# Optimization experiments

Hardware: AMD Instinct MI355X
Metric: run time of the kernel (lower is better)

Reference implementation:

```python
import jax, jax.numpy as jnp
import numpy as np

D_STATE = 16
D_CONV = 4


def layer_norm(x, g, b, eps=1e-5):
    mu = jnp.mean(x, axis=-1, keepdims=True)
    var = jnp.mean(jnp.square(x - mu), axis=-1, keepdims=True)
    return (x - mu) * jax.lax.rsqrt(var + eps) * g + b


def silu(x):
    return x * jax.nn.sigmoid(x)


def mamba(x, in_w, conv_w, conv_b, xproj_w, dt_w, dt_b, Alog, Dp, out_w):
    # x: [B, L, d_model]; in_w: [2*di, d_model]; conv_w: [di, d_conv]
    Bsz, L, _ = x.shape
    di = Dp.shape[0]
    xz = jnp.einsum('bld,ed->ble', x, in_w)          # [B,L,2*di]
    xs, z = jnp.split(xz, 2, axis=-1)
    # causal depthwise conv over L
    xt = xs.transpose(0, 2, 1)                        # [B,di,L]
    xt = jax.lax.conv_general_dilated(
        xt, conv_w[:, None, :], (1,), [(D_CONV - 1, 0)],
        feature_group_count=di, dimension_numbers=('NCH', 'OIH', 'NCH'))
    xs = silu((xt + conv_b[None, :, None]).transpose(0, 2, 1))  # [B,L,di]
    # input-dependent dt, B, C
    dbl = jnp.einsum('bld,ed->ble', xs, xproj_w)      # [B,L,dt_rank+2*ds]
    dt_rank = dt_w.shape[1]
    dt, Bc, Cc = jnp.split(dbl, [dt_rank, dt_rank + D_STATE], axis=-1)
    dt = jax.nn.softplus(jnp.einsum('blr,dr->bld', dt, dt_w) + dt_b)  # [B,L,di]
    A = -jnp.exp(Alog)                                # [di,ds]
    dA = jnp.exp(dt[..., None] * A)                   # [B,L,di,ds]
    dBx = dt[..., None] * Bc[:, :, None, :] * xs[..., None]  # [B,L,di,ds]

    def step(h, inp):
        dA_t, dBx_t, C_t = inp                        # [B,di,ds],[B,di,ds],[B,ds]
        h = dA_t * h + dBx_t
        y = jnp.einsum('bds,bs->bd', h, C_t)
        return h, y

    h0 = jnp.zeros((Bsz, di, D_STATE), x.dtype)
    _, ys = jax.lax.scan(step, h0, (dA.transpose(1, 0, 2, 3),
                                    dBx.transpose(1, 0, 2, 3),
                                    Cc.transpose(1, 0, 2)))
    y = ys.transpose(1, 0, 2) + Dp * xs               # [B,L,di]
    y = y * silu(z)
    return jnp.einsum('bld,od->blo', y, out_w)        # [B,L,d_model]


def _make_mamba_params(key, d_model, scale=0.02):
    di = 2 * d_model
    dt_rank = (d_model + 15) // 16
    ks = jax.random.split(key, 7)
    in_w = jax.random.normal(ks[0], (2 * di, d_model), jnp.float32) * scale
    conv_w = jax.random.normal(ks[1], (di, D_CONV), jnp.float32) * scale
    conv_b = jnp.zeros((di,), jnp.float32)
    xproj_w = jax.random.normal(ks[2], (dt_rank + 2 * D_STATE, di), jnp.float32) * scale
    dt_w = jax.random.normal(ks[3], (di, dt_rank), jnp.float32) * scale
    dt_b = jax.random.uniform(ks[4], (di,), jnp.float32, -5.0, -2.0)
    Alog = jnp.log(jnp.tile(jnp.arange(1, D_STATE + 1, dtype=jnp.float32), (di, 1)))
    Dp = jnp.ones((di,), jnp.float32)
    out_w = jax.random.normal(ks[5], (d_model, di), jnp.float32) * scale
    return in_w, conv_w, conv_b, xproj_w, dt_w, dt_b, Alog, Dp, out_w


def setup_inputs() -> dict:
    key = jax.random.key(0)
    B, L, D = 4, 2048, 1024
    DFF = 4 * D
    ks = jax.random.split(key, 8)
    x = jax.random.normal(ks[0], (B, L, D), jnp.float32)
    m1 = _make_mamba_params(ks[1], D)
    m2 = _make_mamba_params(ks[2], D)
    names1 = ['m1_in_w', 'm1_conv_w', 'm1_conv_b', 'm1_xproj_w', 'm1_dt_w', 'm1_dt_b', 'm1_Alog', 'm1_D', 'm1_out_w']
    names2 = ['m2_in_w', 'm2_conv_w', 'm2_conv_b', 'm2_xproj_w', 'm2_dt_w', 'm2_dt_b', 'm2_Alog', 'm2_D', 'm2_out_w']
    inp = {'x': x}
    inp.update(dict(zip(names1, m1)))
    inp.update(dict(zip(names2, m2)))
    inp['norm_g'] = jnp.ones((D,), jnp.float32)
    inp['norm_b'] = jnp.zeros((D,), jnp.float32)
    inp['ffn_g'] = jnp.ones((D,), jnp.float32)
    inp['ffn_b'] = jnp.zeros((D,), jnp.float32)
    inp['ff1_w'] = jax.random.normal(ks[3], (DFF, D), jnp.float32) * 0.02
    inp['ff1_b'] = jnp.zeros((DFF,), jnp.float32)
    inp['ff2_w'] = jax.random.normal(ks[4], (D, DFF), jnp.float32) * 0.02
    inp['ff2_b'] = jnp.zeros((D,), jnp.float32)
    return inp


def reference(x,
              m1_in_w, m1_conv_w, m1_conv_b, m1_xproj_w, m1_dt_w, m1_dt_b, m1_Alog, m1_D, m1_out_w,
              m2_in_w, m2_conv_w, m2_conv_b, m2_xproj_w, m2_dt_w, m2_dt_b, m2_Alog, m2_D, m2_out_w,
              norm_g, norm_b, ffn_g, ffn_b, ff1_w, ff1_b, ff2_w, ff2_b):
    # BiDirectionalAddBlock (dropout/droppath = identity in eval)
    h = layer_norm(x, norm_g, norm_b)
    fwd = mamba(h, m1_in_w, m1_conv_w, m1_conv_b, m1_xproj_w, m1_dt_w, m1_dt_b, m1_Alog, m1_D, m1_out_w)
    bwd = mamba(h[:, ::-1], m2_in_w, m2_conv_w, m2_conv_b, m2_xproj_w, m2_dt_w, m2_dt_b, m2_Alog, m2_D, m2_out_w)
    block_out = jax.nn.gelu(fwd + bwd + x, approximate=False)  # note: original does NOT flip bwd back
    x = x + block_out
    # FeedForward
    hf = layer_norm(x, ffn_g, ffn_b)
    hf = jax.nn.gelu(jnp.einsum('bld,hd->blh', hf, ff1_w) + ff1_b, approximate=False)
    x = x + jnp.einsum('blh,dh->bld', hf, ff2_w) + ff2_b
    return x
```

## Files before the change

### kernel.cpp

```cpp
#include <hip/hip_runtime.h>
#include <cmath>


namespace {

using u16 = unsigned short;
using uint = unsigned int;

constexpr int kB = 4;
constexpr int kL = 2048;
constexpr int kD = 1024;
constexpr int kDI = 2048;
constexpr int kDFF = 4096;
constexpr int kDS = 16;
constexpr int kDtRank = 64;
constexpr int kNPad = 128;
constexpr int kM = kB * kL;
constexpr int kNCH = 64;

typedef short bf16x8 __attribute__((ext_vector_type(8)));
typedef float f32x4  __attribute__((ext_vector_type(4)));

__device__ __forceinline__ float bf2f(u16 u) {
  union { unsigned int i; float f; } c; c.i = ((unsigned int)u) << 16; return c.f;
}
__device__ __forceinline__ u16 f2bf(float f) {
  union { float f; unsigned int i; } c; c.f = f;
  return (u16)((c.i + 0x7FFFu + ((c.i >> 16) & 1u)) >> 16);
}
__device__ __forceinline__ float geluf(float v) {
  return 0.5f * v * (1.f + erff(v * 0.70710678118654752f));
}
__device__ __forceinline__ float softplusf(float v) {
  return (v > 0.f) ? (v + log1pf(__expf(-v))) : log1pf(__expf(v));
}
__device__ __forceinline__ float siluf(float v) {
  return v / (1.f + __expf(-v));
}
__device__ __forceinline__ float exp2_fast(float v) {
  return __builtin_amdgcn_exp2f(v);
}

__device__ __forceinline__ void async16(const u16* g, u16* l) {
  __builtin_amdgcn_global_load_lds(
      (const __attribute__((address_space(1))) uint*)g,
      (__attribute__((address_space(3))) uint*)l, 16, 0, 0);
}

__global__ __launch_bounds__(256) void ln_kernel(
    const float* __restrict__ x, const float* __restrict__ g,
    const float* __restrict__ b, u16* __restrict__ out) {
  const int row = blockIdx.x;
  const int tid = threadIdx.x;
  const float4 v = ((const float4*)(x + (size_t)row * kD))[tid];
  float s  = v.x + v.y + v.z + v.w;
  float ss = v.x * v.x + v.y * v.y + v.z * v.z + v.w * v.w;
  #pragma unroll
  for (int off = 32; off; off >>= 1) {
    s  += __shfl_xor(s, off);
    ss += __shfl_xor(ss, off);
  }
  __shared__ float ls[4], lss[4];
  const int wid = tid >> 6;
  if ((tid & 63) == 0) { ls[wid] = s; lss[wid] = ss; }
  __syncthreads();
  s  = ls[0] + ls[1] + ls[2] + ls[3];
  ss = lss[0] + lss[1] + lss[2] + lss[3];
  const float mu  = s * (1.f / kD);
  const float inv = rsqrtf(ss * (1.f / kD) - mu * mu + 1e-5f);
  const float4 gg = ((const float4*)g)[tid];
  const float4 bb = ((const float4*)b)[tid];
  ushort4 o;
  o.x = f2bf((v.x - mu) * inv * gg.x + bb.x);
  o.y = f2bf((v.y - mu) * inv * gg.y + bb.y);
  o.z = f2bf((v.z - mu) * inv * gg.z + bb.z);
  o.w = f2bf((v.w - mu) * inv * gg.w + bb.w);
  ((ushort4*)(out + (size_t)row * kD))[tid] = o;
}

__global__ __launch_bounds__(256) void cvt_kernel(
    const float* __restrict__ s, u16* __restrict__ d) {
  const int i = blockIdx.x * 256 + threadIdx.x;
  const float4 v = ((const float4*)s)[i];
  ushort4 o = { f2bf(v.x), f2bf(v.y), f2bf(v.z), f2bf(v.w) };
  ((ushort4*)d)[i] = o;
}

__global__ __launch_bounds__(256) void cvt_xproj_kernel(
    const float* __restrict__ s, u16* __restrict__ d) {
  const int i = blockIdx.x * 256 + threadIdx.x;
  const int r = (i * 4) / kDI;
  ushort4 o = {0, 0, 0, 0};
  if (r < kDtRank + 2 * kDS) {
    const float4 v = ((const float4*)s)[i];
    o.x = f2bf(v.x); o.y = f2bf(v.y); o.z = f2bf(v.z); o.w = f2bf(v.w);
  }
  ((ushort4*)d)[i] = o;
}

template <int ACT, bool BIAS, bool ACC, bool OUTBF, bool REV, bool AMAP,
          bool CMAP>
__global__ __launch_bounds__(256) void gemm_mfma(
    const u16* __restrict__ A, int lda,
    const u16* __restrict__ W, int ldw,
    void* __restrict__ Cp, int ldc, int K,
    const float* __restrict__ bias, int seg_len, int row_off) {
  __shared__ __align__(16) u16 As[128][64];
  __shared__ __align__(16) u16 Ws[128][64];
  const int tid  = threadIdx.x;
  const int bm   = blockIdx.x * 128;
  const int bn   = blockIdx.y * 128;
  const int lane = tid & 63;
  const int wv   = tid >> 6;
  const int wm   = (wv >> 1) * 64;
  const int wn   = (wv & 1) * 64;
  const int l15  = lane & 15;
  const int quad = lane >> 4;
  const int srow = lane >> 3;
  const int swz  = ((lane & 7) ^ srow) * 8;
  const int jx   = (l15 & 7) * 16;

  int ab = 0, all0 = bm;
  if (AMAP || CMAP) {
    ab = bm / seg_len;
    all0 = bm - ab * seg_len;
  }

  int arowv[4];
  #pragma unroll
  for (int it = 0; it < 4; it++) {
    const int rl = it * 32 + wv * 8 + srow;
    if (AMAP) {
      arowv[it] = REV ? (ab * kL + kL - 1 - row_off - all0 - rl)
                      : (ab * kL + row_off + all0 + rl);
    } else {
      arowv[it] = bm + rl;
    }
  }

  f32x4 acc[4][4];
  #pragma unroll
  for (int i = 0; i < 4; i++)
    #pragma unroll
    for (int j = 0; j < 4; j++) acc[i][j] = (f32x4){0.f, 0.f, 0.f, 0.f};

  for (int k0 = 0; k0 < K; k0 += 64) {
    #pragma unroll
    for (int it = 0; it < 4; it++) {
      const int rl = it * 32 + wv * 8 + srow;
      async16(A + (size_t)arowv[it] * lda + k0 + swz, &As[it * 32 + wv * 8][0]);
      async16(W + (size_t)(bn + rl) * ldw + k0 + swz, &Ws[it * 32 + wv * 8][0]);
    }
    __syncthreads();
    #pragma unroll
    for (int ks = 0; ks < 64; ks += 32) {
      const int cb = ((ks >> 3) + quad) * 16;
      bf16x8 af[4], wf[4];
      #pragma unroll
      for (int i = 0; i < 4; i++)
        af[i] = *(const bf16x8*)((const char*)&As[wm + i * 16 + l15][0] +
                                 (cb ^ jx));
      #pragma unroll
      for (int j = 0; j < 4; j++)
        wf[j] = *(const bf16x8*)((const char*)&Ws[wn + j * 16 + l15][0] +
                                 (cb ^ jx));
      #pragma unroll
      for (int i = 0; i < 4; i++)
        #pragma unroll
        for (int j = 0; j < 4; j++)
          acc[i][j] = __builtin_amdgcn_mfma_f32_16x16x32_bf16(
              af[i], wf[j], acc[i][j], 0, 0, 0);
    }
    __syncthreads();
  }

  #pragma unroll
  for (int i = 0; i < 4; i++) {
    #pragma unroll
    for (int j = 0; j < 4; j++) {
      const int col = bn + wn + j * 16 + l15;
      #pragma unroll
      for (int r = 0; r < 4; r++) {
        const int rl2 = wm + i * 16 + quad * 4 + r;
        const int crow = CMAP ? (ab * kL + row_off + all0 + rl2) : (bm + rl2);
        float v = acc[i][j][r];
        if (BIAS) v += bias[col];
        if (ACT == 1) v = softplusf(v);
        if (ACT == 2) v = geluf(v);
        if (OUTBF) {
          ((u16*)Cp)[(size_t)crow * ldc + col] = f2bf(v);
        } else {
          float* p = (float*)Cp + (size_t)crow * ldc + col;
          if (ACC) *p = *p + v; else *p = v;
        }
      }
    }
  }
}

__global__ __launch_bounds__(256) void conv_silu_kernel(
    const u16* __restrict__ xz, const float* __restrict__ w,
    const float* __restrict__ cb, u16* __restrict__ xs,
    const u16* __restrict__ tail_in, u16* __restrict__ tail_out,
    int seg_len, int row_off) {
  const int t = blockIdx.x * 256 + threadIdx.x;
  const int c = t & (kDI - 1);
  const int r = t >> 11;
  const int b = r / seg_len;
  const int ll = r - b * seg_len;
  const int tpos = row_off + ll;

  const float xv0 = bf2f(xz[(size_t)r * (2 * kDI) + c]);
  float acc = cb[c] + w[c * 4 + 3] * xv0;
  #pragma unroll
  for (int j = 1; j <= 3; j++) {
    if (tpos - j >= 0) {
      float xp;
      if (ll - j >= 0) {
        xp = bf2f(xz[(size_t)(r - j) * (2 * kDI) + c]);
      } else {
        xp = bf2f(tail_in[(b * 3 + (3 + ll - j)) * kDI + c]);
      }
      acc += w[c * 4 + 3 - j] * xp;
    }
  }
  xs[(size_t)r * kDI + c] = f2bf(siluf(acc));
  if (ll >= seg_len - 3) {
    tail_out[(b * 3 + (ll - (seg_len - 3))) * kDI + c] = f2bf(xv0);
  }
}

__global__ __launch_bounds__(256, 8) void scan_phaseA(
    const u16* __restrict__ dt, const u16* __restrict__ xs,
    const u16* __restrict__ dbl, const float* __restrict__ Alog,
    float* __restrict__ Pbuf, float* __restrict__ Hbuf,
    int Lseg, int Lc) {
  __shared__ float Bls[32][16];
  const int tid = threadIdx.x;
  const int c = blockIdx.x * 256 + tid;
  const int k = blockIdx.y;
  const int b = blockIdx.z;
  const int base = b * Lseg + k * Lc;
  for (int idx = tid; idx < Lc * 16; idx += 256) {
    const int r = idx >> 4, j = idx & 15;
    Bls[r][j] = bf2f(dbl[(size_t)(base + r) * kNPad + kDtRank + j]);
  }
  __syncthreads();
  float Ac[16], h[16];
  float dtsum = 0.f;
  #pragma unroll
  for (int s = 0; s < 16; s++) {
    Ac[s] = -__expf(Alog[c * kDS + s]) * 1.44269504088896f;
    h[s] = 0.f;
  }
  for (int r = 0; r < Lc; r++) {
    const size_t row = (size_t)(base + r);
    const float dtv = bf2f(dt[row * kDI + c]);
    const float dtx = dtv * bf2f(xs[row * kDI + c]);
    dtsum += dtv;
    const float4* Brow = (const float4*)Bls[r];
    #pragma unroll
    for (int s4 = 0; s4 < 4; s4++) {
      const float4 Bv = Brow[s4];
      const float bb[4] = {Bv.x, Bv.y, Bv.z, Bv.w};
      #pragma unroll
      for (int q = 0; q < 4; q++) {
        const int s = s4 * 4 + q;
        const float dA = exp2_fast(dtv * Ac[s]);
        h[s] = dA * h[s] + dtx * bb[q];
      }
    }
  }
  const size_t o = (((size_t)b * kNCH + k) * kDI + c) * 16;
  #pragma unroll
  for (int s4 = 0; s4 < 4; s4++) {
    *(float4*)&Pbuf[o + s4 * 4] =
        make_float4(exp2_fast(Ac[s4 * 4 + 0] * dtsum),
                    exp2_fast(Ac[s4 * 4 + 1] * dtsum),
                    exp2_fast(Ac[s4 * 4 + 2] * dtsum),
                    exp2_fast(Ac[s4 * 4 + 3] * dtsum));
    *(float4*)&Hbuf[o + s4 * 4] =
        make_float4(h[s4 * 4], h[s4 * 4 + 1], h[s4 * 4 + 2], h[s4 * 4 + 3]);
  }
}

__global__ __launch_bounds__(256) void scan_phaseB(
    float* __restrict__ Pbuf, const float* __restrict__ Hbuf,
    float* __restrict__ hstate, int first) {
  const int t = blockIdx.x * 256 + threadIdx.x;
  const int s = t & 15;
  const int c = (t >> 4) & (kDI - 1);
  const int b = t >> 15;
  float cur = first ? 0.f : hstate[t];
  for (int k = 0; k < kNCH; k++) {
    const size_t idx = (((size_t)b * kNCH + k) * kDI + c) * 16 + s;
    const float p = Pbuf[idx];
    const float hl = Hbuf[idx];
    Pbuf[idx] = cur;
    cur = p * cur + hl;
  }
  hstate[t] = cur;
}

__global__ __launch_bounds__(256, 8) void scan_phaseC(
    const u16* __restrict__ dt, u16* __restrict__ xs,
    const u16* __restrict__ dbl, const u16* __restrict__ xz,
    const float* __restrict__ Alog, const float* __restrict__ Dp,
    const float* __restrict__ Pbuf, int Lseg, int Lc) {
  __shared__ float BC[32][32];
  const int tid = threadIdx.x;
  const int c = blockIdx.x * 256 + tid;
  const int k = blockIdx.y;
  const int b = blockIdx.z;
  const int base = b * Lseg + k * Lc;
  for (int idx = tid; idx < Lc * 32; idx += 256) {
    const int r = idx >> 5, j = idx & 31;
    BC[r][j] = bf2f(dbl[(size_t)(base + r) * kNPad + kDtRank + j]);
  }
  __syncthreads();
  float Ac[16], h[16];
  const size_t o = (((size_t)b * kNCH + k) * kDI + c) * 16;
  #pragma unroll
  for (int s4 = 0; s4 < 4; s4++) {
    const float4 hv = *(const float4*)&Pbuf[o + s4 * 4];
    h[s4 * 4 + 0] = hv.x; h[s4 * 4 + 1] = hv.y;
    h[s4 * 4 + 2] = hv.z; h[s4 * 4 + 3] = hv.w;
  }
  #pragma unroll
  for (int s = 0; s < 16; s++)
    Ac[s] = -__expf(Alog[c * kDS + s]) * 1.44269504088896f;
  const float Dv = Dp[c];
  for (int r = 0; r < Lc; r++) {
    const size_t row = (size_t)(base + r);
    const float dtv = bf2f(dt[row * kDI + c]);
    const float xv = bf2f(xs[row * kDI + c]);
    const float dtx = dtv * xv;
    float y = 0.f;
    const float4* Brow = (const float4*)BC[r];
    const float4* Crow = (const float4*)&BC[r][16];
    #pragma unroll
    for (int s4 = 0; s4 < 4; s4++) {
      const float4 Bv = Brow[s4];
      const float4 Cv = Crow[s4];
      const float bb[4] = {Bv.x, Bv.y, Bv.z, Bv.w};
      const float cc[4] = {Cv.x, Cv.y, Cv.z, Cv.w};
      #pragma unroll
      for (int q = 0; q < 4; q++) {
        const int s = s4 * 4 + q;
        const float dA = exp2_fast(dtv * Ac[s]);
        h[s] = dA * h[s] + dtx * bb[q];
        y += h[s] * cc[q];
      }
    }
    const float z = bf2f(xz[row * (2 * kDI) + kDI + c]);
    xs[row * kDI + c] = f2bf((y + Dv * xv) * siluf(z));
  }
}

__global__ __launch_bounds__(256) void combine_kernel(
    const float* __restrict__ x, float* __restrict__ out) {
  const size_t i = (size_t)blockIdx.x * 256 + threadIdx.x;
  const float4 xv = ((const float4*)x)[i];
  const float4 bv = ((const float4*)out)[i];
  float4 o;
  o.x = xv.x + geluf(bv.x + xv.x);
  o.y = xv.y + geluf(bv.y + xv.y);
  o.z = xv.z + geluf(bv.z + xv.z);
  o.w = xv.w + geluf(bv.w + xv.w);
  ((float4*)out)[i] = o;
}

}

extern "C" void kernel_launch(void* const* d_in, const int* in_sizes, int n_in,
                              void* d_out, int out_size, void* d_ws,
                              size_t ws_size, hipStream_t stream) {
  const float* x = (const float*)d_in[0];
  const float* in_w[2]    = {(const float*)d_in[1],  (const float*)d_in[10]};
  const float* conv_w[2]  = {(const float*)d_in[2],  (const float*)d_in[11]};
  const float* conv_b[2]  = {(const float*)d_in[3],  (const float*)d_in[12]};
  const float* xproj_w[2] = {(const float*)d_in[4],  (const float*)d_in[13]};
  const float* dt_w[2]    = {(const float*)d_in[5],  (const float*)d_in[14]};
  const float* dt_b[2]    = {(const float*)d_in[6],  (const float*)d_in[15]};
  const float* Alog[2]    = {(const float*)d_in[7],  (const float*)d_in[16]};
  const float* Dp[2]      = {(const float*)d_in[8],  (const float*)d_in[17]};
  const float* out_w[2]   = {(const float*)d_in[9],  (const float*)d_in[18]};
  const float* norm_g = (const float*)d_in[19];
  const float* norm_b = (const float*)d_in[20];
  const float* ffn_g  = (const float*)d_in[21];
  const float* ffn_b  = (const float*)d_in[22];
  const float* ff1_w  = (const float*)d_in[23];
  const float* ff1_b  = (const float*)d_in[24];
  const float* ff2_w  = (const float*)d_in[25];
  const float* ff2_b  = (const float*)d_in[26];
  float* out = (float*)d_out;

  constexpr size_t kWCache =
      2 * ((size_t)4096 * kD + (size_t)kD * kDI + (size_t)kNPad * kDI +
           (size_t)kDI * kDtRank) * 2 +
      ((size_t)kDFF * kD + (size_t)kD * kDFF) * 2;
  auto need = [](int nseg) -> size_t {
    const size_t mseg = (size_t)kM / nseg;
    size_t sz = kWCache + 4096;
    sz += (size_t)kM * kD * 2;
    sz += mseg * 4096 * 2;
    sz += mseg * 2048 * 2;
    sz += mseg * 128 * 2;
    sz += mseg * 2048 * 2;
    sz += 2 * (size_t)kB * kNCH * kDI * kDS * 4;
    sz += (size_t)kB * kDI * kDS * 4;
    sz += 2 * (size_t)kB * 3 * kDI * 2;
    sz += 32 * 256;
    return sz;
  };
  int nseg = 1;
  while (nseg <= 16 && need(nseg) > ws_size) nseg *= 2;
  if (nseg > 16) return;
  const int Lseg = kL / nseg;
  const int Mseg = kM / nseg;
  const int Lc = Lseg / kNCH;

  char* base = (char*)d_ws;
  size_t off = 0;
  auto alloc = [&](size_t bytes) {
    char* p = base + off;
    off = (off + bytes + 255) & ~(size_t)255;
    return p;
  };
  u16* w_in[2], *w_out[2], *w_xp[2], *w_dt[2];
  for (int m = 0; m < 2; m++) {
    w_in[m]  = (u16*)alloc((size_t)4096 * kD * 2);
    w_out[m] = (u16*)alloc((size_t)kD * kDI * 2);
    w_xp[m]  = (u16*)alloc((size_t)kNPad * kDI * 2);
    w_dt[m]  = (u16*)alloc((size_t)kDI * kDtRank * 2);
  }
  u16* w_f1 = (u16*)alloc((size_t)kDFF * kD * 2);
  u16* w_f2 = (u16*)alloc((size_t)kD * kDFF * 2);
  u16*   h      = (u16*)alloc((size_t)kM * kD * 2);
  u16*   xz     = (u16*)alloc((size_t)Mseg * 4096 * 2);
  u16*   xs     = (u16*)alloc((size_t)Mseg * 2048 * 2);
  u16*   dbl    = (u16*)alloc((size_t)Mseg * 128 * 2);
  u16*   dtb    = (u16*)alloc((size_t)Mseg * 2048 * 2);
  float* Pbuf   = (float*)alloc((size_t)kB * kNCH * kDI * kDS * 4);
  float* Hbuf   = (float*)alloc((size_t)kB * kNCH * kDI * kDS * 4);
  float* hstate = (float*)alloc((size_t)kB * kDI * kDS * 4);
  u16*   tail0  = (u16*)alloc((size_t)kB * 3 * kDI * 2);
  u16*   tail1  = (u16*)alloc((size_t)kB * 3 * kDI * 2);

  for (int m = 0; m < 2; m++) {
    cvt_kernel<<<(4096 * kD) / 1024, 256, 0, stream>>>(in_w[m], w_in[m]);
    cvt_kernel<<<(kD * kDI) / 1024, 256, 0, stream>>>(out_w[m], w_out[m]);
    cvt_xproj_kernel<<<(kNPad * kDI) / 1024, 256, 0, stream>>>(xproj_w[m],
                                                               w_xp[m]);
    cvt_kernel<<<(kDI * kDtRank) / 1024, 256, 0, stream>>>(dt_w[m], w_dt[m]);
  }
  cvt_kernel<<<(kDFF * kD) / 1024, 256, 0, stream>>>(ff1_w, w_f1);
  cvt_kernel<<<(kD * kDFF) / 1024, 256, 0, stream>>>(ff2_w, w_f2);

  ln_kernel<<<kM, 256, 0, stream>>>(x, norm_g, norm_b, h);

  for (int m = 0; m < 2; m++) {
    for (int s = 0; s < nseg; s++) {
      const int l0 = s * Lseg;
      u16* tin  = (s & 1) ? tail0 : tail1;
      u16* tout = (s & 1) ? tail1 : tail0;
      if (m == 0)
        gemm_mfma<0, false, false, true, false, true, false>
            <<<dim3(Mseg / 128, 4096 / 128), 256, 0, stream>>>(
                h, kD, w_in[m], kD, xz, 4096, kD, nullptr, Lseg, l0);
      else
        gemm_mfma<0, false, false, true, true, true, false>
            <<<dim3(Mseg / 128, 4096 / 128), 256, 0, stream>>>(
                h, kD, w_in[m], kD, xz, 4096, kD, nullptr, Lseg, l0);
      conv_silu_kernel<<<(Mseg * kDI) / 256, 256, 0, stream>>>(
          xz, conv_w[m], conv_b[m], xs, tin, tout, Lseg, l0);
      gemm_mfma<0, false, false, true, false, false, false>
          <<<dim3(Mseg / 128, 1), 256, 0, stream>>>(
              xs, kDI, w_xp[m], kDI, dbl, kNPad, kDI, nullptr, Lseg, l0);
      gemm_mfma<1, true, false, true, false, false, false>
          <<<dim3(Mseg / 128, kDI / 128), 256, 0, stream>>>(
              dbl, kNPad, w_dt[m], kDtRank, dtb, kDI, kDtRank, dt_b[m],
              Lseg, l0);
      scan_phaseA<<<dim3(kDI / 256, kNCH, kB), 256, 0, stream>>>(
          dtb, xs, dbl, Alog[m], Pbuf, Hbuf, Lseg, Lc);
      scan_phaseB<<<(kB * kDI * kDS) / 256, 256, 0, stream>>>(
          Pbuf, Hbuf, hstate, (s == 0) ? 1 : 0);
      scan_phaseC<<<dim3(kDI / 256, kNCH, kB), 256, 0, stream>>>(
          dtb, xs, dbl, xz, Alog[m], Dp[m], Pbuf, Lseg, Lc);
      if (m == 0)
        gemm_mfma<0, false, false, false, false, false, true>
            <<<dim3(Mseg / 128, kD / 128), 256, 0, stream>>>(
                xs, kDI, w_out[m], kDI, out, kD, kDI, nullptr, Lseg, l0);
      else
        gemm_mfma<0, false, true, false, false, false, true>
            <<<dim3(Mseg / 128, kD / 128), 256, 0, stream>>>(
                xs, kDI, w_out[m], kDI, out, kD, kDI, nullptr, Lseg, l0);
    }
  }

  combine_kernel<<<(kM * kD) / 1024, 256, 0, stream>>>(x, out);

  ln_kernel<<<kM, 256, 0, stream>>>(out, ffn_g, ffn_b, h);
  for (int s = 0; s < nseg; s++) {
    const int r0 = s * Mseg;
    gemm_mfma<2, true, false, true, false, true, false>
        <<<dim3(Mseg / 128, kDFF / 128), 256, 0, stream>>>(
            h, kD, w_f1, kD, xz, kDFF, kD, ff1_b, Mseg, r0);
    gemm_mfma<0, true, true, false, false, false, true>
        <<<dim3(Mseg / 128, kD / 128), 256, 0, stream>>>(
            xz, kDFF, w_f2, kDFF, out, kD, kDFF, ff2_b, Mseg, r0);
  }
}
```

Baseline: 1.410 ms.

## Fuse combine with LayerNorm, batch weight conversions, narrow tiles for N=1024 GEMMs

Merges the GELU-residual combine with the FFN LayerNorm into one per-row kernel, which removes a full re-read of the activation buffer. Replaces ten weight-conversion launches with a single multi-job kernel. Adds a TILEN template parameter so the out-projection and FF2 GEMMs (N=1024) use 128x64 tiles, doubling block count for better CU occupancy at the cost of less W-tile reuse per block.

```diff
diff --git a/kernel.cpp b/kernel.cpp
--- a/kernel.cpp
+++ b/kernel.cpp
@@ -78,42 +78,89 @@
   ((ushort4*)(out + (size_t)row * kD))[tid] = o;
 }
 
-__global__ __launch_bounds__(256) void cvt_kernel(
-    const float* __restrict__ s, u16* __restrict__ d) {
-  const int i = blockIdx.x * 256 + threadIdx.x;
-  const float4 v = ((const float4*)s)[i];
-  ushort4 o = { f2bf(v.x), f2bf(v.y), f2bf(v.z), f2bf(v.w) };
-  ((ushort4*)d)[i] = o;
-}
-
-__global__ __launch_bounds__(256) void cvt_xproj_kernel(
-    const float* __restrict__ s, u16* __restrict__ d) {
-  const int i = blockIdx.x * 256 + threadIdx.x;
-  const int r = (i * 4) / kDI;
-  ushort4 o = {0, 0, 0, 0};
-  if (r < kDtRank + 2 * kDS) {
-    const float4 v = ((const float4*)s)[i];
-    o.x = f2bf(v.x); o.y = f2bf(v.y); o.z = f2bf(v.z); o.w = f2bf(v.w);
-  }
-  ((ushort4*)d)[i] = o;
-}
-
-template <int ACT, bool BIAS, bool ACC, bool OUTBF, bool REV, bool AMAP,
-          bool CMAP>
+__global__ __launch_bounds__(256) void combine_ln_kernel(
+    const float* __restrict__ x, float* __restrict__ out,
+    const float* __restrict__ g, const float* __restrict__ b,
+    u16* __restrict__ h) {
+  const int row = blockIdx.x;
+  const int tid = threadIdx.x;
+  const float4 xv = ((const float4*)(x + (size_t)row * kD))[tid];
+  const float4 bv = ((const float4*)(out + (size_t)row * kD))[tid];
+  float4 o;
+  o.x = xv.x + geluf(bv.x + xv.x);
+  o.y = xv.y + geluf(bv.y + xv.y);
+  o.z = xv.z + geluf(bv.z + xv.z);
+  o.w = xv.w + geluf(bv.w + xv.w);
+  ((float4*)(out + (size_t)row * kD))[tid] = o;
+  float s  = o.x + o.y + o.z + o.w;
+  float ss = o.x * o.x + o.y * o.y + o.z * o.z + o.w * o.w;
+  #pragma unroll
+  for (int off = 32; off; off >>= 1) {
+    s  += __shfl_xor(s, off);
+    ss += __shfl_xor(ss, off);
+  }
+  __shared__ float ls[4], lss[4];
+  const int wid = tid >> 6;
+  if ((tid & 63) == 0) { ls[wid] = s; lss[wid] = ss; }
+  __syncthreads();
+  s  = ls[0] + ls[1] + ls[2] + ls[3];
+  ss = lss[0] + lss[1] + lss[2] + lss[3];
+  const float mu  = s * (1.f / kD);
+  const float inv = rsqrtf(ss * (1.f / kD) - mu * mu + 1e-5f);
+  const float4 gg = ((const float4*)g)[tid];
+  const float4 bb = ((const float4*)b)[tid];
+  ushort4 ho;
+  ho.x = f2bf((o.x - mu) * inv * gg.x + bb.x);
+  ho.y = f2bf((o.y - mu) * inv * gg.y + bb.y);
+  ho.z = f2bf((o.z - mu) * inv * gg.z + bb.z);
+  ho.w = f2bf((o.w - mu) * inv * gg.w + bb.w);
+  ((ushort4*)(h + (size_t)row * kD))[tid] = ho;
+}
+
+struct KJob { const float* s; u16* d; int n4; int blk0; int xp; };
+struct KJobs { KJob j[10]; };
+
+__global__ __launch_bounds__(256) void cvt_all_kernel(KJobs J) {
+  const int bi = blockIdx.x;
+  #pragma unroll
+  for (int k = 0; k < 10; k++) {
+    const KJob job = J.j[k];
+    const int nb = (job.n4 + 255) >> 8;
+    if (bi >= job.blk0 && bi < job.blk0 + nb) {
+      const int i = (bi - job.blk0) * 256 + threadIdx.x;
+      if (i < job.n4) {
+        ushort4 o = {0, 0, 0, 0};
+        bool valid = true;
+        if (job.xp) valid = ((i * 4) >> 11) < (kDtRank + 2 * kDS);
+        if (valid) {
+          const float4 v = ((const float4*)job.s)[i];
+          o.x = f2bf(v.x); o.y = f2bf(v.y); o.z = f2bf(v.z); o.w = f2bf(v.w);
+        }
+        ((ushort4*)job.d)[i] = o;
+      }
+      return;
+    }
+  }
+}
+
+template <int TILEN, int ACT, bool BIAS, bool ACC, bool OUTBF, bool REV,
+          bool AMAP, bool CMAP>
 __global__ __launch_bounds__(256) void gemm_mfma(
     const u16* __restrict__ A, int lda,
     const u16* __restrict__ W, int ldw,
     void* __restrict__ Cp, int ldc, int K,
     const float* __restrict__ bias, int seg_len, int row_off) {
+  constexpr int MI = (TILEN == 128) ? 4 : 2;
+  constexpr int WSTR = TILEN / 32;
   __shared__ __align__(16) u16 As[128][64];
-  __shared__ __align__(16) u16 Ws[128][64];
+  __shared__ __align__(16) u16 Ws[TILEN][64];
   const int tid  = threadIdx.x;
   const int bm   = blockIdx.x * 128;
-  const int bn   = blockIdx.y * 128;
+  const int bn   = blockIdx.y * TILEN;
   const int lane = tid & 63;
   const int wv   = tid >> 6;
-  const int wm   = (wv >> 1) * 64;
-  const int wn   = (wv & 1) * 64;
+  const int wm   = (TILEN == 128) ? (wv >> 1) * 64 : wv * 32;
+  const int wn   = (TILEN == 128) ? (wv & 1) * 64 : 0;
   const int l15  = lane & 15;
   const int quad = lane >> 4;
   const int srow = lane >> 3;
@@ -138,9 +185,9 @@
     }
   }
 
-  f32x4 acc[4][4];
-  #pragma unroll
-  for (int i = 0; i < 4; i++)
+  f32x4 acc[MI][4];
+  #pragma unroll
+  for (int i = 0; i < MI; i++)
     #pragma unroll
     for (int j = 0; j < 4; j++) acc[i][j] = (f32x4){0.f, 0.f, 0.f, 0.f};
 
@@ -149,15 +196,19 @@
     for (int it = 0; it < 4; it++) {
       const int rl = it * 32 + wv * 8 + srow;
       async16(A + (size_t)arowv[it] * lda + k0 + swz, &As[it * 32 + wv * 8][0]);
+    }
+    #pragma unroll
+    for (int it = 0; it < WSTR; it++) {
+      const int rl = it * 32 + wv * 8 + srow;
       async16(W + (size_t)(bn + rl) * ldw + k0 + swz, &Ws[it * 32 + wv * 8][0]);
     }
     __syncthreads();
     #pragma unroll
     for (int ks = 0; ks < 64; ks += 32) {
       const int cb = ((ks >> 3) + quad) * 16;
-      bf16x8 af[4], wf[4];
+      bf16x8 af[MI], wf[4];
       #pragma unroll
-      for (int i = 0; i < 4; i++)
+      for (int i = 0; i < MI; i++)
         af[i] = *(const bf16x8*)((const char*)&As[wm + i * 16 + l15][0] +
                                  (cb ^ jx));
       #pragma unroll
@@ -165,7 +216,7 @@
         wf[j] = *(const bf16x8*)((const char*)&Ws[wn + j * 16 + l15][0] +
                                  (cb ^ jx));
       #pragma unroll
-      for (int i = 0; i < 4; i++)
+      for (int i = 0; i < MI; i++)
         #pragma unroll
         for (int j = 0; j < 4; j++)
           acc[i][j] = __builtin_amdgcn_mfma_f32_16x16x32_bf16(
@@ -175,7 +226,7 @@
   }
 
   #pragma unroll
-  for (int i = 0; i < 4; i++) {
+  for (int i = 0; i < MI; i++) {
     #pragma unroll
     for (int j = 0; j < 4; j++) {
       const int col = bn + wn + j * 16 + l15;
@@ -355,19 +406,6 @@
     const float z = bf2f(xz[row * (2 * kDI) + kDI + c]);
     xs[row * kDI + c] = f2bf((y + Dv * xv) * siluf(z));
   }
-}
-
-__global__ __launch_bounds__(256) void combine_kernel(
-    const float* __restrict__ x, float* __restrict__ out) {
-  const size_t i = (size_t)blockIdx.x * 256 + threadIdx.x;
-  const float4 xv = ((const float4*)x)[i];
-  const float4 bv = ((const float4*)out)[i];
-  float4 o;
-  o.x = xv.x + geluf(bv.x + xv.x);
-  o.y = xv.y + geluf(bv.y + xv.y);
-  o.z = xv.z + geluf(bv.z + xv.z);
-  o.w = xv.w + geluf(bv.w + xv.w);
-  ((float4*)out)[i] = o;
 }
 
 }
@@ -447,15 +485,25 @@
   u16*   tail0  = (u16*)alloc((size_t)kB * 3 * kDI * 2);
   u16*   tail1  = (u16*)alloc((size_t)kB * 3 * kDI * 2);
 
-  for (int m = 0; m < 2; m++) {
-    cvt_kernel<<<(4096 * kD) / 1024, 256, 0, stream>>>(in_w[m], w_in[m]);
-    cvt_kernel<<<(kD * kDI) / 1024, 256, 0, stream>>>(out_w[m], w_out[m]);
-    cvt_xproj_kernel<<<(kNPad * kDI) / 1024, 256, 0, stream>>>(xproj_w[m],
-                                                               w_xp[m]);
-    cvt_kernel<<<(kDI * kDtRank) / 1024, 256, 0, stream>>>(dt_w[m], w_dt[m]);
-  }
-  cvt_kernel<<<(kDFF * kD) / 1024, 256, 0, stream>>>(ff1_w, w_f1);
-  cvt_kernel<<<(kD * kDFF) / 1024, 256, 0, stream>>>(ff2_w, w_f2);
+  {
+    KJobs J;
+    int b = 0, ji = 0;
+    auto addjob = [&](const float* s, u16* d, int n4, int xp) {
+      J.j[ji].s = s; J.j[ji].d = d; J.j[ji].n4 = n4;
+      J.j[ji].blk0 = b; J.j[ji].xp = xp;
+      b += (n4 + 255) >> 8;
+      ji++;
+    };
+    for (int m = 0; m < 2; m++) {
+      addjob(in_w[m],  w_in[m],  (4096 * kD) / 4, 0);
+      addjob(out_w[m], w_out[m], (kD * kDI) / 4, 0);
+      addjob(xproj_w[m], w_xp[m], (kNPad * kDI) / 4, 1);
+      addjob(dt_w[m],  w_dt[m],  (kDI * kDtRank) / 4, 0);
+    }
+    addjob(ff1_w, w_f1, (kDFF * kD) / 4, 0);
+    addjob(ff2_w, w_f2, (kD * kDFF) / 4, 0);
+    cvt_all_kernel<<<b, 256, 0, stream>>>(J);
+  }
 
   ln_kernel<<<kM, 256, 0, stream>>>(x, norm_g, norm_b, h);
 
@@ -465,19 +513,19 @@
       u16* tin  = (s & 1) ? tail0 : tail1;
       u16* tout = (s & 1) ? tail1 : tail0;
       if (m == 0)
-        gemm_mfma<0, false, false, true, false, true, false>
+        gemm_mfma<128, 0, false, false, true, false, true, false>
             <<<dim3(Mseg / 128, 4096 / 128), 256, 0, stream>>>(
                 h, kD, w_in[m], kD, xz, 4096, kD, nullptr, Lseg, l0);
       else
-        gemm_mfma<0, false, false, true, true, true, false>
+        gemm_mfma<128, 0, false, false, true, true, true, false>
             <<<dim3(Mseg / 128, 4096 / 128), 256, 0, stream>>>(
                 h, kD, w_in[m], kD, xz, 4096, kD, nullptr, Lseg, l0);
       conv_silu_kernel<<<(Mseg * kDI) / 256, 256, 0, stream>>>(
           xz, conv_w[m], conv_b[m], xs, tin, tout, Lseg, l0);
-      gemm_mfma<0, false, false, true, false, false, false>
+      gemm_mfma<128, 0, false, false, true, false, false, false>
           <<<dim3(Mseg / 128, 1), 256, 0, stream>>>(
               xs, kDI, w_xp[m], kDI, dbl, kNPad, kDI, nullptr, Lseg, l0);
-      gemm_mfma<1, true, false, true, false, false, false>
+      gemm_mfma<128, 1, true, false, true, false, false, false>
           <<<dim3(Mseg / 128, kDI / 128), 256, 0, stream>>>(
               dbl, kNPad, w_dt[m], kDtRank, dtb, kDI, kDtRank, dt_b[m],
               Lseg, l0);
@@ -488,26 +536,25 @@
       scan_phaseC<<<dim3(kDI / 256, kNCH, kB), 256, 0, stream>>>(
           dtb, xs, dbl, xz, Alog[m], Dp[m], Pbuf, Lseg, Lc);
       if (m == 0)
-        gemm_mfma<0, false, false, false, false, false, true>
-            <<<dim3(Mseg / 128, kD / 128), 256, 0, stream>>>(
+        gemm_mfma<64, 0, false, false, false, false, false, true>
+            <<<dim3(Mseg / 128, kD / 64), 256, 0, stream>>>(
                 xs, kDI, w_out[m], kDI, out, kD, kDI, nullptr, Lseg, l0);
       else
-        gemm_mfma<0, false, true, false, false, false, true>
-            <<<dim3(Mseg / 128, kD / 128), 256, 0, stream>>>(
+        gemm_mfma<64, 0, false, true, false, false, false, true>
+            <<<dim3(Mseg / 128, kD / 64), 256, 0, stream>>>(
                 xs, kDI, w_out[m], kDI, out, kD, kDI, nullptr, Lseg, l0);
     }
   }
 
-  combine_kernel<<<(kM * kD) / 1024, 256, 0, stream>>>(x, out);
-
-  ln_kernel<<<kM, 256, 0, stream>>>(out, ffn_g, ffn_b, h);
+  combine_ln_kernel<<<kM, 256, 0, stream>>>(x, out, ffn_g, ffn_b, h);
+
   for (int s = 0; s < nseg; s++) {
     const int r0 = s * Mseg;
-    gemm_mfma<2, true, false, true, false, true, false>
+    gemm_mfma<128, 2, true, false, true, false, true, false>
         <<<dim3(Mseg / 128, kDFF / 128), 256, 0, stream>>>(
             h, kD, w_f1, kD, xz, kDFF, kD, ff1_b, Mseg, r0);
-    gemm_mfma<0, true, true, false, false, false, true>
-        <<<dim3(Mseg / 128, kD / 128), 256, 0, stream>>>(
+    gemm_mfma<64, 0, true, true, false, false, false, true>
+        <<<dim3(Mseg / 128, kD / 64), 256, 0, stream>>>(
             xz, kDFF, w_f2, kDFF, out, kD, kDFF, ff2_b, Mseg, r0);
   }
 }
```

After: 1.371 ms. 2.7% less time.
